# Performance work log

Hardware: AMD Instinct MI355X
Metric: run time of the kernel (lower is better)

The kernel has to match this reference:

```python
import jax, jax.numpy as jnp
import numpy as np

N_EMBEDDING = 512
EMBEDDING_DIM = 64
COMMITMENT_COST = 0.25


def setup_inputs() -> dict:
    key = jax.random.key(0)
    k1, k2 = jax.random.split(key)
    inputs = jax.random.normal(k1, (64, 32, 32, EMBEDDING_DIM), dtype=jnp.float32)
    context = jnp.zeros((1,), dtype=jnp.float32)  # unused by the module
    # variance_scaling(1.0, 'fan_in', 'uniform') on shape (D, K): fan_in = D
    limit = np.sqrt(3.0 / EMBEDDING_DIM)
    embeddings = jax.random.uniform(
        k2, (EMBEDDING_DIM, N_EMBEDDING), dtype=jnp.float32,
        minval=-limit, maxval=limit)
    return {"inputs": inputs, "context": context, "embeddings": embeddings}


def reference(inputs, context, embeddings):
    D, K = embeddings.shape
    flat = inputs.reshape(-1, D)  # [N, D]
    distances = (
        jnp.sum(jnp.square(flat), axis=1, keepdims=True)
        - 2.0 * jnp.matmul(flat, embeddings)
        + jnp.sum(jnp.square(embeddings), axis=0, keepdims=True)
    )
    encoding_indices_flat = jnp.argmax(-distances, axis=1)  # [N]
    encodings = jax.nn.one_hot(encoding_indices_flat, K, dtype=distances.dtype)
    encoding_indices = encoding_indices_flat.reshape(inputs.shape[:-1])
    # gather codebook rows: embeddings.T is [K, D]
    quantized = embeddings.T[encoding_indices]  # [B, H, W, D]

    e_latent_loss = jnp.mean(jnp.square(jax.lax.stop_gradient(quantized) - inputs))
    q_latent_loss = jnp.mean(jnp.square(quantized - jax.lax.stop_gradient(inputs)))
    loss = q_latent_loss + COMMITMENT_COST * e_latent_loss

    # straight-through estimator
    quantized = inputs + jax.lax.stop_gradient(quantized - inputs)

    avg_probs = jnp.mean(encodings, axis=0)
    perplexity = jnp.exp(-jnp.sum(avg_probs * jnp.log(avg_probs + 1e-10)))
    return (quantized, loss, perplexity, encodings, encoding_indices, distances)
```

## Files before the change

kernel.cpp:

```cpp
#include <hip/hip_runtime.h>


#define NROWS 65536
#define DIM 64
#define KCODES 512
#define ROWS_PER_BLOCK 64
#define NBLOCKS (NROWS / ROWS_PER_BLOCK)
#define RPW 8

#define QUANT_OFF 0ull
#define LOSS_OFF  4194304ull
#define PERP_OFF  4194305ull
#define ENC_OFF   4194306ull
#define IDX_OFF   37748738ull
#define DIST_OFF  37814274ull

typedef float f32x4 __attribute__((ext_vector_type(4)));

__global__ __launch_bounds__(64) void vq_transpose(
    const float* __restrict__ emb, float* __restrict__ et)
{
    const int t = blockIdx.x * 64 + threadIdx.x;
    f32x4* et4 = (f32x4*)et;
#pragma unroll
    for (int dq = 0; dq < 16; ++dq) {
        f32x4 v;
        v.x = emb[(dq * 4 + 0) * KCODES + t];
        v.y = emb[(dq * 4 + 1) * KCODES + t];
        v.z = emb[(dq * 4 + 2) * KCODES + t];
        v.w = emb[(dq * 4 + 3) * KCODES + t];
        et4[t * 16 + dq] = v;
    }
}

__global__ __launch_bounds__(512, 4) void vq_main(
    const float* __restrict__ inp, const float* __restrict__ emb,
    const float* __restrict__ et,
    float* __restrict__ out, int* __restrict__ hist,
    float* __restrict__ loss_part)
{
    __shared__ f32x4 s_X[ROWS_PER_BLOCK * 16];
    __shared__ float s_sumx2[ROWS_PER_BLOCK];
    __shared__ float s_loss[8];

    const int tid  = threadIdx.x;
    const int w    = tid >> 6;
    const int lane = tid & 63;
    const int rbase = blockIdx.x * ROWS_PER_BLOCK;
    const int rl0  = w * RPW;

    {
        const f32x4* inp4 = (const f32x4*)inp + (size_t)blockIdx.x * 1024;
        s_X[tid]       = inp4[tid];
        s_X[512 + tid] = inp4[512 + tid];
    }
    __syncthreads();

    {
        const int row_l = w * RPW + (lane >> 3);
        const int q = lane & 7;
        const f32x4 a = s_X[row_l * 16 + q * 2 + 0];
        const f32x4 b = s_X[row_l * 16 + q * 2 + 1];
        float p = 0.f;
        p = fmaf(a.x, a.x, p); p = fmaf(a.y, a.y, p);
        p = fmaf(a.z, a.z, p); p = fmaf(a.w, a.w, p);
        p = fmaf(b.x, b.x, p); p = fmaf(b.y, b.y, p);
        p = fmaf(b.z, b.z, p); p = fmaf(b.w, b.w, p);
        p += __shfl_xor(p, 1);
        p += __shfl_xor(p, 2);
        p += __shfl_xor(p, 4);
        if (q == 0) s_sumx2[row_l] = p;
    }

    float bd[RPW];
    int   ck[RPW];
#pragma unroll
    for (int r = 0; r < RPW; ++r) { bd[r] = 3.4e38f; ck[r] = 0x7fffffff; }

    const float* ebase = emb + lane * 4;
    float loss_acc = 0.f;

    auto pass = [&](auto hc) {
        constexpr int H = decltype(hc)::value;
        f32x4 acc[RPW];
#pragma unroll
        for (int r = 0; r < RPW; ++r) acc[r] = (f32x4){0.f, 0.f, 0.f, 0.f};
        f32x4 se = {0.f, 0.f, 0.f, 0.f};

#pragma unroll 1
        for (int dq = 0; dq < 16; ++dq) {
            f32x4 e4[4];
#pragma unroll
            for (int sub = 0; sub < 4; ++sub)
                e4[sub] = *(const f32x4*)(ebase + (dq * 4 + sub) * KCODES
                                          + H * 256);
#pragma unroll
            for (int sub = 0; sub < 4; ++sub)
                se = se + e4[sub] * e4[sub];
#pragma unroll
            for (int r = 0; r < RPW; ++r) {
                const f32x4 xv = s_X[(rl0 + r) * 16 + dq];
                acc[r] = acc[r] + xv.x * e4[0];
                acc[r] = acc[r] + xv.y * e4[1];
                acc[r] = acc[r] + xv.z * e4[2];
                acc[r] = acc[r] + xv.w * e4[3];
            }
        }

        const f32x4 zero = {0.f, 0.f, 0.f, 0.f};
#pragma unroll
        for (int r = 0; r < RPW; ++r) {
            const int row = rbase + rl0 + r;
            const f32x4 dd = (se + s_sumx2[rl0 + r]) + (-2.f) * acc[r];

            f32x4* dp = (f32x4*)(out + DIST_OFF) + (size_t)row * 128;
            __builtin_nontemporal_store(dd, dp + H * 64 + lane);
            f32x4* ep = (f32x4*)(out + ENC_OFF) + (size_t)row * 128;
            __builtin_nontemporal_store(zero, ep + H * 64 + lane);

            const float m = fminf(fminf(dd.x, dd.y), fminf(dd.z, dd.w));
            int j = 3;
            if (dd.z == m) j = 2;
            if (dd.y == m) j = 1;
            if (dd.x == m) j = 0;
            const int kk = H * 256 + lane * 4 + j;
            if (m < bd[r] || (m == bd[r] && kk < ck[r])) {
                bd[r] = m;
                ck[r] = kk;
            }
        }
    };

    const int first = ((w >> 2) ^ blockIdx.x) & 1;
    if (first == 0) {
        pass(std::integral_constant<int, 0>{});
        pass(std::integral_constant<int, 1>{});
    } else {
        pass(std::integral_constant<int, 1>{});
        pass(std::integral_constant<int, 0>{});
    }

    const f32x4* et4 = (const f32x4*)et;

#pragma unroll
    for (int r = 0; r < RPW; ++r) {
        const int row = rbase + rl0 + r;

        float fd = bd[r];
#pragma unroll
        for (int off = 32; off; off >>= 1)
            fd = fminf(fd, __shfl_xor(fd, off));
        int c2 = (bd[r] == fd) ? ck[r] : 0x7fffffff;
#pragma unroll
        for (int off = 32; off; off >>= 1) {
            const int ok = __shfl_xor(c2, off);
            c2 = ok < c2 ? ok : c2;
        }

        const int slot = c2 >> 2;
        if (lane == (slot & 63)) {
            f32x4 v;
            v.x = (c2 & 3) == 0 ? 1.f : 0.f;
            v.y = (c2 & 3) == 1 ? 1.f : 0.f;
            v.z = (c2 & 3) == 2 ? 1.f : 0.f;
            v.w = (c2 & 3) == 3 ? 1.f : 0.f;
            f32x4* ep = (f32x4*)(out + ENC_OFF) + (size_t)row * 128;
            __builtin_nontemporal_store(v, ep + slot);
        }

        if (lane < 16) {
            const f32x4 q = et4[c2 * 16 + lane];
            ((f32x4*)(out + QUANT_OFF + (size_t)row * DIM))[lane] = q;
        }

        if (lane == 0) {
            out[IDX_OFF + row] = (float)c2;
            atomicAdd(&hist[c2], 1);
            loss_acc += fd;
        }
    }

    if (lane == 0) s_loss[w] = loss_acc;
    __syncthreads();
    if (tid == 0) {
        float s = 0.f;
#pragma unroll
        for (int i = 0; i < 8; ++i) s += s_loss[i];
        loss_part[blockIdx.x] = s;
    }
}

__global__ __launch_bounds__(512) void vq_final(
    const int* __restrict__ hist, const float* __restrict__ loss_part,
    float* __restrict__ out)
{
    __shared__ float s_red[8];
    __shared__ float s_red2[8];
    const int tid = threadIdx.x;
    const int w = tid >> 6, lane = tid & 63;

    float p = (float)hist[tid] * (1.f / 65536.f);
    float t = p * logf(p + 1e-10f);
    float l = loss_part[tid] + loss_part[tid + 512];
#pragma unroll
    for (int off = 32; off; off >>= 1) {
        t += __shfl_xor(t, off);
        l += __shfl_xor(l, off);
    }
    if (lane == 0) { s_red[w] = t; s_red2[w] = l; }
    __syncthreads();
    if (tid == 0) {
        float s = 0.f, ls = 0.f;
#pragma unroll
        for (int i = 0; i < 8; ++i) { s += s_red[i]; ls += s_red2[i]; }
        out[PERP_OFF] = expf(-s);
        out[LOSS_OFF] = ls * (1.25f / 4194304.f);
    }
}

extern "C" void kernel_launch(void* const* d_in, const int* in_sizes, int n_in,
                              void* d_out, int out_size, void* d_ws, size_t ws_size,
                              hipStream_t stream) {
    const float* inp = (const float*)d_in[0];
    const float* emb = (const float*)d_in[2];
    float* out = (float*)d_out;
    int*   hist      = (int*)d_ws;
    float* loss_part = (float*)((char*)d_ws + 2048);
    float* et        = (float*)((char*)d_ws + 8192);

    (void)hipMemsetAsync(d_ws, 0, 2048, stream);
    vq_transpose<<<dim3(8), dim3(64), 0, stream>>>(emb, et);
    vq_main<<<dim3(NBLOCKS), dim3(512), 0, stream>>>(
        inp, emb, et, out, hist, loss_part);
    vq_final<<<dim3(1), dim3(512), 0, stream>>>(hist, loss_part, out);
}
```

Baseline: 114.3 us.

## Split codebook halves across blocks, stage codebook in LDS, use packed FMA

The main kernel now gives each 64-row group two blocks, one per codebook half. Each block stages its half of the codebook in shared memory and computes the dot products with inline v_pk_fma_f32. Each block writes a per-row packed (distance, index) minimum via 64-bit atomicMin, and a new post kernel then does the quantized gather, one-hot write, histogram and loss. Codebook norms are precomputed in the transpose kernel. This aims to raise parallelism and cut global codebook reloads, at the cost of an extra launch, a 512KB memset, atomics and swapping nontemporal stores for ordinary ones.

```diff
diff --git a/kernel.cpp b/kernel.cpp
--- a/kernel.cpp
+++ b/kernel.cpp
@@ -4,9 +4,6 @@
 #define NROWS 65536
 #define DIM 64
 #define KCODES 512
-#define ROWS_PER_BLOCK 64
-#define NBLOCKS (NROWS / ROWS_PER_BLOCK)
-#define RPW 8
 
 #define QUANT_OFF 0ull
 #define LOSS_OFF  4194304ull
@@ -16,12 +13,22 @@
 #define DIST_OFF  37814274ull
 
 typedef float f32x4 __attribute__((ext_vector_type(4)));
+typedef float f32x2 __attribute__((ext_vector_type(2)));
+
+#define PKFMA_LO(a, e, x) \
+    asm("v_pk_fma_f32 %0, %1, %2, %0 op_sel:[0,0,0] op_sel_hi:[1,0,1]" \
+        : "+v"(a) : "v"(e), "v"(x))
+#define PKFMA_HI(a, e, x) \
+    asm("v_pk_fma_f32 %0, %1, %2, %0 op_sel:[0,1,0] op_sel_hi:[1,1,1]" \
+        : "+v"(a) : "v"(e), "v"(x))
 
 __global__ __launch_bounds__(64) void vq_transpose(
-    const float* __restrict__ emb, float* __restrict__ et)
+    const float* __restrict__ emb, float* __restrict__ et,
+    float* __restrict__ se)
 {
     const int t = blockIdx.x * 64 + threadIdx.x;
     f32x4* et4 = (f32x4*)et;
+    float s = 0.f;
 #pragma unroll
     for (int dq = 0; dq < 16; ++dq) {
         f32x4 v;
@@ -30,37 +37,50 @@
         v.z = emb[(dq * 4 + 2) * KCODES + t];
         v.w = emb[(dq * 4 + 3) * KCODES + t];
         et4[t * 16 + dq] = v;
-    }
+        s = fmaf(v.x, v.x, s); s = fmaf(v.y, v.y, s);
+        s = fmaf(v.z, v.z, s); s = fmaf(v.w, v.w, s);
+    }
+    se[t] = s;
 }
 
 __global__ __launch_bounds__(512, 4) void vq_main(
     const float* __restrict__ inp, const float* __restrict__ emb,
-    const float* __restrict__ et,
-    float* __restrict__ out, int* __restrict__ hist,
-    float* __restrict__ loss_part)
-{
-    __shared__ f32x4 s_X[ROWS_PER_BLOCK * 16];
-    __shared__ float s_sumx2[ROWS_PER_BLOCK];
-    __shared__ float s_loss[8];
+    const float* __restrict__ se,
+    float* __restrict__ out, unsigned long long* __restrict__ minpack)
+{
+    __shared__ f32x4 s_E[64 * 64];
+    __shared__ f32x4 s_X[64 * 16];
 
     const int tid  = threadIdx.x;
     const int w    = tid >> 6;
     const int lane = tid & 63;
-    const int rbase = blockIdx.x * ROWS_PER_BLOCK;
-    const int rl0  = w * RPW;
+    const int rg   = blockIdx.x >> 1;
+    const int h    = blockIdx.x & 1;
+    const int rbase = rg * 64;
+    const int rl0   = w * 8;
 
     {
-        const f32x4* inp4 = (const f32x4*)inp + (size_t)blockIdx.x * 1024;
+        const f32x4* e4g = (const f32x4*)emb;
+#pragma unroll
+        for (int i = 0; i < 8; ++i) {
+            const int idx = i * 512 + tid;
+            const int d = idx >> 6, c = idx & 63;
+            s_E[idx] = e4g[d * 128 + h * 64 + c];
+        }
+    }
+    {
+        const f32x4* inp4 = (const f32x4*)inp + (size_t)rg * 1024;
         s_X[tid]       = inp4[tid];
         s_X[512 + tid] = inp4[512 + tid];
     }
     __syncthreads();
 
+    float sx[8];
     {
-        const int row_l = w * RPW + (lane >> 3);
-        const int q = lane & 7;
-        const f32x4 a = s_X[row_l * 16 + q * 2 + 0];
-        const f32x4 b = s_X[row_l * 16 + q * 2 + 1];
+        const int rr = lane >> 3;
+        const int q  = lane & 7;
+        const f32x4 a = s_X[(rl0 + rr) * 16 + q * 2 + 0];
+        const f32x4 b = s_X[(rl0 + rr) * 16 + q * 2 + 1];
         float p = 0.f;
         p = fmaf(a.x, a.x, p); p = fmaf(a.y, a.y, p);
         p = fmaf(a.z, a.z, p); p = fmaf(a.w, a.w, p);
@@ -69,117 +89,118 @@
         p += __shfl_xor(p, 1);
         p += __shfl_xor(p, 2);
         p += __shfl_xor(p, 4);
-        if (q == 0) s_sumx2[row_l] = p;
-    }
-
-    float bd[RPW];
-    int   ck[RPW];
-#pragma unroll
-    for (int r = 0; r < RPW; ++r) { bd[r] = 3.4e38f; ck[r] = 0x7fffffff; }
-
-    const float* ebase = emb + lane * 4;
-    float loss_acc = 0.f;
-
-    auto pass = [&](auto hc) {
-        constexpr int H = decltype(hc)::value;
-        f32x4 acc[RPW];
-#pragma unroll
-        for (int r = 0; r < RPW; ++r) acc[r] = (f32x4){0.f, 0.f, 0.f, 0.f};
-        f32x4 se = {0.f, 0.f, 0.f, 0.f};
-
-#pragma unroll 1
-        for (int dq = 0; dq < 16; ++dq) {
-            f32x4 e4[4];
-#pragma unroll
-            for (int sub = 0; sub < 4; ++sub)
-                e4[sub] = *(const f32x4*)(ebase + (dq * 4 + sub) * KCODES
-                                          + H * 256);
-#pragma unroll
-            for (int sub = 0; sub < 4; ++sub)
-                se = se + e4[sub] * e4[sub];
-#pragma unroll
-            for (int r = 0; r < RPW; ++r) {
-                const f32x4 xv = s_X[(rl0 + r) * 16 + dq];
-                acc[r] = acc[r] + xv.x * e4[0];
-                acc[r] = acc[r] + xv.y * e4[1];
-                acc[r] = acc[r] + xv.z * e4[2];
-                acc[r] = acc[r] + xv.w * e4[3];
-            }
-        }
-
-        const f32x4 zero = {0.f, 0.f, 0.f, 0.f};
-#pragma unroll
-        for (int r = 0; r < RPW; ++r) {
-            const int row = rbase + rl0 + r;
-            const f32x4 dd = (se + s_sumx2[rl0 + r]) + (-2.f) * acc[r];
-
-            f32x4* dp = (f32x4*)(out + DIST_OFF) + (size_t)row * 128;
-            __builtin_nontemporal_store(dd, dp + H * 64 + lane);
-            f32x4* ep = (f32x4*)(out + ENC_OFF) + (size_t)row * 128;
-            __builtin_nontemporal_store(zero, ep + H * 64 + lane);
-
-            const float m = fminf(fminf(dd.x, dd.y), fminf(dd.z, dd.w));
-            int j = 3;
-            if (dd.z == m) j = 2;
-            if (dd.y == m) j = 1;
-            if (dd.x == m) j = 0;
-            const int kk = H * 256 + lane * 4 + j;
-            if (m < bd[r] || (m == bd[r] && kk < ck[r])) {
-                bd[r] = m;
-                ck[r] = kk;
-            }
-        }
-    };
-
-    const int first = ((w >> 2) ^ blockIdx.x) & 1;
-    if (first == 0) {
-        pass(std::integral_constant<int, 0>{});
-        pass(std::integral_constant<int, 1>{});
-    } else {
-        pass(std::integral_constant<int, 1>{});
-        pass(std::integral_constant<int, 0>{});
-    }
-
-    const f32x4* et4 = (const f32x4*)et;
-
-#pragma unroll
-    for (int r = 0; r < RPW; ++r) {
+#pragma unroll
+        for (int r = 0; r < 8; ++r) sx[r] = __shfl(p, r * 8);
+    }
+
+    const f32x4 se4 = ((const f32x4*)se)[h * 64 + lane];
+
+    f32x2 acc[8][2];
+#pragma unroll
+    for (int r = 0; r < 8; ++r) {
+        acc[r][0] = (f32x2){0.f, 0.f};
+        acc[r][1] = (f32x2){0.f, 0.f};
+    }
+
+#pragma unroll 2
+    for (int dq = 0; dq < 16; ++dq) {
+        f32x4 e4[4];
+#pragma unroll
+        for (int sub = 0; sub < 4; ++sub)
+            e4[sub] = s_E[(dq * 4 + sub) * 64 + lane];
+        f32x2 elo[4], ehi[4];
+#pragma unroll
+        for (int sub = 0; sub < 4; ++sub) {
+            elo[sub] = __builtin_shufflevector(e4[sub], e4[sub], 0, 1);
+            ehi[sub] = __builtin_shufflevector(e4[sub], e4[sub], 2, 3);
+        }
+#pragma unroll
+        for (int r = 0; r < 8; ++r) {
+            const f32x4 xv = s_X[(rl0 + r) * 16 + dq];
+            const f32x2 xlo = __builtin_shufflevector(xv, xv, 0, 1);
+            const f32x2 xhi = __builtin_shufflevector(xv, xv, 2, 3);
+            PKFMA_LO(acc[r][0], elo[0], xlo);
+            PKFMA_LO(acc[r][1], ehi[0], xlo);
+            PKFMA_HI(acc[r][0], elo[1], xlo);
+            PKFMA_HI(acc[r][1], ehi[1], xlo);
+            PKFMA_LO(acc[r][0], elo[2], xhi);
+            PKFMA_LO(acc[r][1], ehi[2], xhi);
+            PKFMA_HI(acc[r][0], elo[3], xhi);
+            PKFMA_HI(acc[r][1], ehi[3], xhi);
+        }
+    }
+
+    const f32x4 zero = {0.f, 0.f, 0.f, 0.f};
+#pragma unroll
+    for (int r = 0; r < 8; ++r) {
         const int row = rbase + rl0 + r;
-
-        float fd = bd[r];
+        const f32x4 a = {acc[r][0].x, acc[r][0].y, acc[r][1].x, acc[r][1].y};
+        const f32x4 dd = (se4 + sx[r]) + (-2.f) * a;
+
+        f32x4* dp = (f32x4*)(out + DIST_OFF) + (size_t)row * 128 + h * 64;
+        dp[lane] = dd;
+        f32x4* ep = (f32x4*)(out + ENC_OFF) + (size_t)row * 128 + h * 64;
+        ep[lane] = zero;
+
+        float fd = fminf(fminf(dd.x, dd.y), fminf(dd.z, dd.w));
 #pragma unroll
         for (int off = 32; off; off >>= 1)
             fd = fminf(fd, __shfl_xor(fd, off));
-        int c2 = (bd[r] == fd) ? ck[r] : 0x7fffffff;
-#pragma unroll
-        for (int off = 32; off; off >>= 1) {
-            const int ok = __shfl_xor(c2, off);
-            c2 = ok < c2 ? ok : c2;
-        }
-
-        const int slot = c2 >> 2;
-        if (lane == (slot & 63)) {
-            f32x4 v;
-            v.x = (c2 & 3) == 0 ? 1.f : 0.f;
-            v.y = (c2 & 3) == 1 ? 1.f : 0.f;
-            v.z = (c2 & 3) == 2 ? 1.f : 0.f;
-            v.w = (c2 & 3) == 3 ? 1.f : 0.f;
-            f32x4* ep = (f32x4*)(out + ENC_OFF) + (size_t)row * 128;
-            __builtin_nontemporal_store(v, ep + slot);
-        }
-
-        if (lane < 16) {
-            const f32x4 q = et4[c2 * 16 + lane];
-            ((f32x4*)(out + QUANT_OFF + (size_t)row * DIM))[lane] = q;
-        }
+
+        int c2 = 0x7fffffff;
+        unsigned long long m;
+        m = __ballot(dd.x == fd);
+        if (m) { int c = (int)__builtin_ctzll(m) * 4 + 0; c2 = c < c2 ? c : c2; }
+        m = __ballot(dd.y == fd);
+        if (m) { int c = (int)__builtin_ctzll(m) * 4 + 1; c2 = c < c2 ? c : c2; }
+        m = __ballot(dd.z == fd);
+        if (m) { int c = (int)__builtin_ctzll(m) * 4 + 2; c2 = c < c2 ? c : c2; }
+        m = __ballot(dd.w == fd);
+        if (m) { int c = (int)__builtin_ctzll(m) * 4 + 3; c2 = c < c2 ? c : c2; }
 
         if (lane == 0) {
-            out[IDX_OFF + row] = (float)c2;
-            atomicAdd(&hist[c2], 1);
-            loss_acc += fd;
-        }
-    }
-
+            unsigned ub = __float_as_uint(fd);
+            ub = (ub & 0x80000000u) ? ~ub : (ub | 0x80000000u);
+            const unsigned long long pk =
+                ((unsigned long long)ub << 32) | (unsigned)(h * 256 + c2);
+            atomicMin(&minpack[row], pk);
+        }
+    }
+}
+
+__global__ __launch_bounds__(512) void vq_post(
+    const unsigned long long* __restrict__ minpack,
+    const float* __restrict__ et,
+    float* __restrict__ out, int* __restrict__ hist,
+    float* __restrict__ loss_part)
+{
+    __shared__ float s_loss[8];
+    const int tid = threadIdx.x;
+    const int w = tid >> 6, lane = tid & 63;
+    const int sub = lane & 15;
+    const int rq  = lane >> 4;
+    const f32x4* et4 = (const f32x4*)et;
+    float loss_acc = 0.f;
+
+#pragma unroll
+    for (int it = 0; it < 4; ++it) {
+        const int row = blockIdx.x * 128 + w * 16 + it * 4 + rq;
+        const unsigned long long pk = minpack[row];
+        const int k = (int)(pk & 0xFFFFFFFFull);
+
+        ((f32x4*)(out + QUANT_OFF + (size_t)row * DIM))[sub] = et4[k * 16 + sub];
+
+        if (sub == 0) {
+            out[IDX_OFF + row] = (float)k;
+            out[ENC_OFF + (size_t)row * KCODES + k] = 1.f;
+            atomicAdd(&hist[k], 1);
+            unsigned ub = (unsigned)(pk >> 32);
+            const unsigned fb = (ub & 0x80000000u) ? (ub ^ 0x80000000u) : ~ub;
+            loss_acc += __uint_as_float(fb);
+        }
+    }
+    loss_acc += __shfl_xor(loss_acc, 16);
+    loss_acc += __shfl_xor(loss_acc, 32);
     if (lane == 0) s_loss[w] = loss_acc;
     __syncthreads();
     if (tid == 0) {
@@ -201,7 +222,7 @@
 
     float p = (float)hist[tid] * (1.f / 65536.f);
     float t = p * logf(p + 1e-10f);
-    float l = loss_part[tid] + loss_part[tid + 512];
+    float l = loss_part[tid];
 #pragma unroll
     for (int off = 32; off; off >>= 1) {
         t += __shfl_xor(t, off);
@@ -226,11 +247,15 @@
     float* out = (float*)d_out;
     int*   hist      = (int*)d_ws;
     float* loss_part = (float*)((char*)d_ws + 2048);
-    float* et        = (float*)((char*)d_ws + 8192);
+    float* se        = (float*)((char*)d_ws + 4096);
+    unsigned long long* minpack =
+        (unsigned long long*)((char*)d_ws + 8192);
+    float* et        = (float*)((char*)d_ws + 8192 + 524288);
 
     (void)hipMemsetAsync(d_ws, 0, 2048, stream);
-    vq_transpose<<<dim3(8), dim3(64), 0, stream>>>(emb, et);
-    vq_main<<<dim3(NBLOCKS), dim3(512), 0, stream>>>(
-        inp, emb, et, out, hist, loss_part);
+    (void)hipMemsetAsync(minpack, 0xFF, (size_t)NROWS * 8, stream);
+    vq_transpose<<<dim3(8), dim3(64), 0, stream>>>(emb, et, se);
+    vq_main<<<dim3(2048), dim3(512), 0, stream>>>(inp, emb, se, out, minpack);
+    vq_post<<<dim3(512), dim3(512), 0, stream>>>(minpack, et, out, hist, loss_part);
     vq_final<<<dim3(1), dim3(512), 0, stream>>>(hist, loss_part, out);
 }
```

Result: slower. 134.5 us (+17.6%).
